# Kernel tuning notes

Hardware: AMD Instinct MI355X
Metric: run time of the kernel (lower is better)

## Reference

```python
import jax, jax.numpy as jnp
import numpy as np

NUM_HEADS = 8
DIM = 256
MLP_RATIO = 1.2


def conv1x1(x, w, b=None):
    # x: [B,C,H,W], w: [O,C]
    y = jnp.einsum('bchw,oc->bohw', x, w)
    if b is not None:
        y = y + b[None, :, None, None]
    return y


def dwconv3x3(x, w):
    # depthwise 3x3, stride 1, padding 1. w: [C,1,3,3]
    C = x.shape[1]
    return jax.lax.conv_general_dilated(
        x, w, window_strides=(1, 1), padding=((1, 1), (1, 1)),
        dimension_numbers=('NCHW', 'OIHW', 'NCHW'), feature_group_count=C)


def l2norm(x, axis):
    # matches torch.nn.functional.normalize (eps=1e-12 clamp on the norm)
    n = jnp.sqrt(jnp.sum(x * x, axis=axis, keepdims=True))
    return x / jnp.maximum(n, 1e-12)


def setup_inputs() -> dict:
    key = jax.random.key(0)
    ks = jax.random.split(key, 7)
    dim = DIM
    hidden = int(dim * MLP_RATIO)  # 307
    B, H, W = 8, 64, 64
    return {
        'x': jax.random.normal(ks[0], (B, dim, H, W), jnp.float32),
        'w_qkv': jax.random.normal(ks[1], (3 * dim, dim), jnp.float32) * 0.02,
        'w_dw': jax.random.normal(ks[2], (3 * dim, 1, 3, 3), jnp.float32) * 0.1,
        'temperature': jnp.ones((NUM_HEADS, 1, 1), jnp.float32),
        'w_proj': jax.random.normal(ks[3], (dim, dim), jnp.float32) * 0.02,
        'w_mlp1': jax.random.normal(ks[4], (hidden, dim), jnp.float32) * 0.02,
        'b_mlp1': jnp.zeros((hidden,), jnp.float32),
        'w_mlp2': jax.random.normal(ks[5], (dim, hidden), jnp.float32) * 0.02,
        'b_mlp2': jnp.zeros((dim,), jnp.float32),
    }


def reference(x, w_qkv, w_dw, temperature, w_proj, w_mlp1, b_mlp1, w_mlp2, b_mlp2):
    b, c, h, w = x.shape
    head = NUM_HEADS
    # MDTA attention: qkv 1x1 conv -> depthwise 3x3 conv
    qkv = dwconv3x3(conv1x1(x, w_qkv), w_dw)          # [B,3C,H,W]
    q, k, v = jnp.split(qkv, 3, axis=1)
    to_heads = lambda t: t.reshape(b, head, c // head, h * w)  # b head c (h w)
    q, k, v = to_heads(q), to_heads(k), to_heads(v)
    q = l2norm(q, -1)
    k = l2norm(k, -1)
    # channel-wise (transposed) attention: [B,head,c_h,c_h]
    attn = jnp.einsum('bhcn,bhdn->bhcd', q, k) * temperature[None]
    attn = jax.nn.softmax(attn, axis=-1)
    out = jnp.einsum('bhcd,bhdn->bhcn', attn, v).reshape(b, c, h, w)
    x = x + conv1x1(out, w_proj)                       # residual 1
    # conv-FFN (1x1 -> GELU -> 1x1) with residual
    y = jax.nn.gelu(conv1x1(x, w_mlp1, b_mlp1))
    x = x + conv1x1(y, w_mlp2, b_mlp2)                 # residual 2
    return x
```

## Files before the change

kernel.cpp:

```cpp
#include <hip/hip_runtime.h>
#include <hip/hip_bf16.h>
#include <math.h>

typedef __hip_bfloat16 bf16;
using s16x8 = __attribute__((ext_vector_type(8))) short;
using f32x4 = __attribute__((ext_vector_type(4))) float;

#define B_ 8
#define C_ 256
#define HW_ 4096
#define TC_ 768
#define NH_ 8
#define CH_ 32
#define HID_ 307
#define HIDP_ 320
#define HIDM_ 384

__device__ __forceinline__ float ldf(const float* p) { return *p; }
__device__ __forceinline__ float ldf(const bf16* p)  { return __bfloat162float(*p); }
__device__ __forceinline__ void  stf(float* p, float v) { *p = v; }
__device__ __forceinline__ void  stf(bf16* p, float v)  { *p = __float2bfloat16(v); }

__device__ __forceinline__ float gelu_tanh(float u) {
    float c = 0.7978845608028654f * (u + 0.044715f * u * u * u);
    return 0.5f * u * (1.f + tanhf(c));
}

__device__ __forceinline__ void stage16(const void* g, uint32_t* lbase, int lane) {
#if __has_builtin(__builtin_amdgcn_global_load_lds)
    __builtin_amdgcn_global_load_lds(
        (const __attribute__((address_space(1))) uint32_t*)g,
        (__attribute__((address_space(3))) uint32_t*)lbase, 16, 0, 0);
#else
    ((uint4*)lbase)[lane] = *(const uint4*)g;
#endif
}

template <typename TOut>
__global__ __launch_bounds__(256) void mfma_gemm(
    const bf16* __restrict__ A, const bf16* __restrict__ Xt,
    const float* __restrict__ bias, const float* __restrict__ res,
    TOut* __restrict__ out, int M, int N, int Kp, int act,
    size_t astride, size_t xstride, size_t ostride)
{
    int bt = blockIdx.z;
    A  += (size_t)bt * astride;
    Xt += (size_t)bt * xstride;
    out += (size_t)bt * ostride;
    if (res) res += (size_t)bt * ostride;
    int m0 = blockIdx.y * 128, n0 = blockIdx.x * 128;

    __shared__ uint32_t lds[8192];

    int tid = threadIdx.x;
    int w = tid >> 6, lane = tid & 63;
    int wr = w >> 1, wc = w & 1;
    int r15 = lane & 15, g = lane >> 4;

    f32x4 zero4 = {0.f, 0.f, 0.f, 0.f};
    f32x4 acc[4][4];
    #pragma unroll
    for (int i = 0; i < 4; i++)
        #pragma unroll
        for (int j = 0; j < 4; j++) acc[i][j] = zero4;

    int nkt = Kp >> 6;
    for (int kt = 0; kt < nkt; kt++) {
        #pragma unroll
        for (int i = 0; i < 4; i++) {
            int row = (w * 4 + i) * 8 + (lane >> 3);
            int us  = (lane & 7) ^ (row & 7);
            const bf16* sa = A  + (size_t)(m0 + row) * Kp + kt * 64 + us * 8;
            const bf16* sb = Xt + (size_t)(n0 + row) * Kp + kt * 64 + us * 8;
            stage16(sa, &lds[(w * 4 + i) * 256], lane);
            stage16(sb, &lds[4096 + (w * 4 + i) * 256], lane);
        }
        __syncthreads();

        s16x8 af[4][2], bfr[4][2];
        #pragma unroll
        for (int mm = 0; mm < 4; mm++) {
            int r = wr * 64 + mm * 16 + r15;
            #pragma unroll
            for (int ks = 0; ks < 2; ks++) {
                int u = (ks * 4 + g) ^ (r & 7);
                af[mm][ks] = *(const s16x8*)&lds[(unsigned)(r * 8 + u) * 4];
            }
        }
        #pragma unroll
        for (int nn = 0; nn < 4; nn++) {
            int r = wc * 64 + nn * 16 + r15;
            #pragma unroll
            for (int ks = 0; ks < 2; ks++) {
                int u = (ks * 4 + g) ^ (r & 7);
                bfr[nn][ks] = *(const s16x8*)&lds[4096 + (unsigned)(r * 8 + u) * 4];
            }
        }

        #pragma unroll
        for (int ks = 0; ks < 2; ks++)
            #pragma unroll
            for (int mm = 0; mm < 4; mm++)
                #pragma unroll
                for (int nn = 0; nn < 4; nn++)
                    acc[mm][nn] = __builtin_amdgcn_mfma_f32_16x16x32_bf16(
                        af[mm][ks], bfr[nn][ks], acc[mm][nn], 0, 0, 0);
        __syncthreads();
    }

    #pragma unroll
    for (int mm = 0; mm < 4; mm++) {
        int mbase = m0 + wr * 64 + mm * 16 + g * 4;
        #pragma unroll
        for (int rr = 0; rr < 4; rr++) {
            int m = mbase + rr;
            if (m >= M) continue;
            float bv = bias ? bias[m] : 0.f;
            #pragma unroll
            for (int nn = 0; nn < 4; nn++) {
                int n = n0 + wc * 64 + nn * 16 + r15;
                float v = acc[mm][nn][rr] + bv;
                if (act == 1) v = gelu_tanh(v);
                if (res) v += res[(size_t)m * N + n];
                stf(&out[(size_t)m * N + n], v);
            }
        }
    }
}

template <typename TIn>
__global__ __launch_bounds__(256) void transpose_kernel(
    const TIn* __restrict__ in, bf16* __restrict__ out,
    int R, int Ncols, int Rpad, size_t in_z, size_t out_z)
{
    in  += (size_t)blockIdx.z * in_z;
    out += (size_t)blockIdx.z * out_z;
    __shared__ float t[32][33];
    int r0 = blockIdx.y * 32, n0 = blockIdx.x * 32;
    int tx = threadIdx.x & 31, ty = threadIdx.x >> 5;
    #pragma unroll
    for (int s = 0; s < 4; s++) {
        int r = r0 + ty + 8 * s;
        t[ty + 8 * s][tx] = (r < R) ? ldf(&in[(size_t)r * Ncols + n0 + tx]) : 0.f;
    }
    __syncthreads();
    #pragma unroll
    for (int s = 0; s < 4; s++) {
        int n = n0 + ty + 8 * s;
        out[(size_t)n * Rpad + r0 + tx] = __float2bfloat16(t[tx][ty + 8 * s]);
    }
}

__global__ __launch_bounds__(256) void convert_pad_kernel(
    const float* __restrict__ in, bf16* __restrict__ out,
    int R, int Cin, int Cout)
{
    int c = blockIdx.x * 256 + threadIdx.x;
    int r = blockIdx.y;
    if (c >= Cout) return;
    float v = (r < R && c < Cin) ? in[(size_t)r * Cin + c] : 0.f;
    out[(size_t)r * Cout + c] = __float2bfloat16(v);
}

__global__ __launch_bounds__(256) void dwconv_kernel(
    const bf16* __restrict__ in, const float* __restrict__ wdw,
    bf16* __restrict__ out)
{
    size_t gid = (size_t)blockIdx.x * 256 + threadIdx.x;
    int pix  = (int)(gid & 4095);
    int xcol = pix & 63, yrow = pix >> 6;
    size_t plane = gid >> 12;
    int c = (int)(plane % TC_);
    const bf16* ip = in + (plane << 12);

    float wv[9];
    #pragma unroll
    for (int t = 0; t < 9; t++) wv[t] = wdw[c * 9 + t];

    float acc = 0.f;
    #pragma unroll
    for (int dy = -1; dy <= 1; dy++) {
        int yy = yrow + dy;
        if (yy < 0 || yy > 63) continue;
        #pragma unroll
        for (int dx = -1; dx <= 1; dx++) {
            int xx = xcol + dx;
            if (xx < 0 || xx > 63) continue;
            acc += wv[(dy + 1) * 3 + (dx + 1)] * __bfloat162float(ip[yy * 64 + xx]);
        }
    }
    out[gid] = __float2bfloat16(acc);
}

__global__ void zero_kernel(float* __restrict__ p, int n)
{
    int i = blockIdx.x * 256 + threadIdx.x;
    if (i < n) p[i] = 0.f;
}

__global__ __launch_bounds__(256) void qk_partial_kernel(
    const bf16* __restrict__ qkv, float* __restrict__ S,
    float* __restrict__ n2q, float* __restrict__ n2k)
{
    int bh = blockIdx.y;
    int b = bh >> 3, h = bh & 7;
    int base = blockIdx.x * 512;
    const bf16* qp = qkv + ((size_t)b * TC_ + h * CH_) * HW_;
    const bf16* kp = qp + (size_t)C_ * HW_;

    __shared__ float qs[32][65], ks[32][65];

    int tid = threadIdx.x;
    int nr = tid >> 3, seg = (tid & 7) * 8;
    float accA[4] = {0.f, 0.f, 0.f, 0.f};
    float sq = 0.f, sk = 0.f;

    for (int t0 = 0; t0 < 512; t0 += 64) {
        #pragma unroll
        for (int i = 0; i < 8; i++) {
            int l = tid + 256 * i;
            int r = l >> 6, cc = l & 63;
            qs[r][cc] = __bfloat162float(qp[(size_t)r * HW_ + base + t0 + cc]);
            ks[r][cc] = __bfloat162float(kp[(size_t)r * HW_ + base + t0 + cc]);
        }
        __syncthreads();
        #pragma unroll
        for (int p = 0; p < 4; p++) {
            int e = tid + 256 * p;
            int i = e >> 5, j = e & 31;
            float s = 0.f;
            #pragma unroll
            for (int kk = 0; kk < 64; kk++) s += qs[i][kk] * ks[j][kk];
            accA[p] += s;
        }
        #pragma unroll
        for (int s = 0; s < 8; s++) {
            float vq = qs[nr][seg + s]; sq += vq * vq;
            float vk = ks[nr][seg + s]; sk += vk * vk;
        }
        __syncthreads();
    }

    #pragma unroll
    for (int off = 1; off < 8; off <<= 1) {
        sq += __shfl_xor(sq, off);
        sk += __shfl_xor(sk, off);
    }
    if ((tid & 7) == 0) {
        atomicAdd(&n2q[bh * 32 + nr], sq);
        atomicAdd(&n2k[bh * 32 + nr], sk);
    }
    #pragma unroll
    for (int p = 0; p < 4; p++) {
        int e = tid + 256 * p;
        atomicAdd(&S[(size_t)bh * 1024 + e], accA[p]);
    }
}

__global__ __launch_bounds__(64) void softmax_kernel(
    const float* __restrict__ S, const float* __restrict__ n2q,
    const float* __restrict__ n2k, const float* __restrict__ temp,
    float* __restrict__ attnb)
{
    int bh = blockIdx.x, h = bh & 7;
    __shared__ float nkl[32];
    int tid = threadIdx.x;
    if (tid < 32) nkl[tid] = fmaxf(sqrtf(n2k[bh * 32 + tid]), 1e-12f);
    __syncthreads();
    if (tid < 32) {
        float nq = fmaxf(sqrtf(n2q[bh * 32 + tid]), 1e-12f);
        float tp = temp[h];
        float row[32];
        float m = -1e30f;
        #pragma unroll
        for (int j = 0; j < 32; j++) {
            row[j] = S[(size_t)bh * 1024 + tid * 32 + j] * tp / (nq * nkl[j]);
            m = fmaxf(m, row[j]);
        }
        float s = 0.f;
        #pragma unroll
        for (int j = 0; j < 32; j++) { row[j] = expf(row[j] - m); s += row[j]; }
        float inv = 1.f / s;
        #pragma unroll
        for (int j = 0; j < 32; j++)
            attnb[(size_t)bh * 1024 + tid * 32 + j] = row[j] * inv;
    }
}

__global__ __launch_bounds__(256) void wcomb_kernel(
    const float* __restrict__ w_proj, const float* __restrict__ attnb,
    bf16* __restrict__ wcomb)
{
    int bh = blockIdx.x;
    int b = bh >> 3, h = bh & 7;
    __shared__ float at[32][33];
    int tid = threadIdx.x;
    #pragma unroll
    for (int p = 0; p < 4; p++) {
        int e = tid + 256 * p;
        at[e >> 5][e & 31] = attnb[(size_t)bh * 1024 + e];
    }
    __syncthreads();
    int m = tid;
    float wrow[32];
    #pragma unroll
    for (int i = 0; i < 32; i++) wrow[i] = w_proj[(size_t)m * C_ + h * 32 + i];
    #pragma unroll
    for (int j = 0; j < 32; j++) {
        float s = 0.f;
        #pragma unroll
        for (int i = 0; i < 32; i++) s += wrow[i] * at[i][j];
        wcomb[((size_t)b * C_ + m) * C_ + h * 32 + j] = __float2bfloat16(s);
    }
}

extern "C" void kernel_launch(void* const* d_in, const int* in_sizes, int n_in,
                              void* d_out, int out_size, void* d_ws, size_t ws_size,
                              hipStream_t stream)
{
    const float* x      = (const float*)d_in[0];
    const float* w_qkv  = (const float*)d_in[1];
    const float* w_dw   = (const float*)d_in[2];
    const float* temp   = (const float*)d_in[3];
    const float* w_proj = (const float*)d_in[4];
    const float* w_mlp1 = (const float*)d_in[5];
    const float* b_mlp1 = (const float*)d_in[6];
    const float* w_mlp2 = (const float*)d_in[7];
    const float* b_mlp2 = (const float*)d_in[8];

    char* ws = (char*)d_ws;
    bf16*  qkv_pre = (bf16*)ws;
    bf16*  xt      = (bf16*)(ws + (size_t)50331648);
    bf16*  wqkv_bf = (bf16*)(ws + (size_t)67108864);
    bf16*  qkv     = (bf16*)(ws + (size_t)50331648);
    float* x2      = (float*)ws;
    float* S_f     = (float*)(ws + (size_t)33554432);
    float* n2q     = S_f + 65536;
    float* n2k     = n2q + 2048;
    float* attnb   = n2k + 2048;
    bf16*  wcomb   = (bf16*)(ws + (size_t)34095104);
    bf16*  wm1_bf  = (bf16*)(ws + (size_t)35143680);
    bf16*  wm2_bf  = (bf16*)(ws + (size_t)35340288);
    bf16*  vt      = (bf16*)(ws + (size_t)35504128);
    bf16*  ybuf    = (bf16*)(ws + (size_t)52281344);
    bf16*  x2t     = (bf16*)(ws + (size_t)72400896);
    bf16*  yt      = (bf16*)(ws + (size_t)72400896);

    convert_pad_kernel<<<dim3(1, TC_), 256, 0, stream>>>(w_qkv, wqkv_bf, TC_, C_, C_);
    transpose_kernel<float><<<dim3(128, 8, B_), 256, 0, stream>>>(
        x, xt, C_, HW_, C_, (size_t)C_ * HW_, (size_t)HW_ * C_);

    mfma_gemm<bf16><<<dim3(32, 6, B_), 256, 0, stream>>>(
        wqkv_bf, xt, nullptr, nullptr, qkv_pre, TC_, HW_, C_, 0,
        0, (size_t)HW_ * C_, (size_t)TC_ * HW_);

    dwconv_kernel<<<(B_ * TC_ * HW_) / 256, 256, 0, stream>>>(qkv_pre, w_dw, qkv);

    zero_kernel<<<(69632 + 255) / 256, 256, 0, stream>>>(S_f, 69632);
    qk_partial_kernel<<<dim3(8, 64), 256, 0, stream>>>(qkv, S_f, n2q, n2k);
    softmax_kernel<<<64, 64, 0, stream>>>(S_f, n2q, n2k, temp, attnb);
    wcomb_kernel<<<64, 256, 0, stream>>>(w_proj, attnb, wcomb);

    convert_pad_kernel<<<dim3(1, HIDM_), 256, 0, stream>>>(w_mlp1, wm1_bf, HID_, C_, C_);
    convert_pad_kernel<<<dim3(2, C_), 256, 0, stream>>>(w_mlp2, wm2_bf, C_, HID_, HIDP_);
    transpose_kernel<bf16><<<dim3(128, 8, B_), 256, 0, stream>>>(
        qkv + (size_t)2 * C_ * HW_, vt, C_, HW_, C_,
        (size_t)TC_ * HW_, (size_t)HW_ * C_);

    mfma_gemm<float><<<dim3(32, 2, B_), 256, 0, stream>>>(
        wcomb, vt, nullptr, x, x2, C_, HW_, C_, 0,
        (size_t)C_ * C_, (size_t)HW_ * C_, (size_t)C_ * HW_);

    transpose_kernel<float><<<dim3(128, 8, B_), 256, 0, stream>>>(
        x2, x2t, C_, HW_, C_, (size_t)C_ * HW_, (size_t)HW_ * C_);

    mfma_gemm<bf16><<<dim3(32, 3, B_), 256, 0, stream>>>(
        wm1_bf, x2t, b_mlp1, nullptr, ybuf, HID_, HW_, C_, 1,
        0, (size_t)HW_ * C_, (size_t)HID_ * HW_);

    transpose_kernel<bf16><<<dim3(128, 10, B_), 256, 0, stream>>>(
        ybuf, yt, HID_, HW_, HIDP_, (size_t)HID_ * HW_, (size_t)HW_ * HIDP_);

    mfma_gemm<float><<<dim3(32, 2, B_), 256, 0, stream>>>(
        wm2_bf, yt, b_mlp2, x2, (float*)d_out, C_, HW_, HIDP_, 0,
        0, (size_t)HW_ * HIDP_, (size_t)C_ * HW_);
}
```

Before: 443.8 us.

## Emit MLP1 output pre-transposed and tile depthwise conv through LDS

```diff
diff --git a/kernel.cpp b/kernel.cpp
--- a/kernel.cpp
+++ b/kernel.cpp
@@ -21,6 +21,10 @@
 __device__ __forceinline__ void  stf(float* p, float v) { *p = v; }
 __device__ __forceinline__ void  stf(bf16* p, float v)  { *p = __float2bfloat16(v); }
 
+__device__ __forceinline__ float bfu2f(unsigned short u) {
+    union { unsigned int i; float f; } c; c.i = ((unsigned int)u) << 16; return c.f;
+}
+
 __device__ __forceinline__ float gelu_tanh(float u) {
     float c = 0.7978845608028654f * (u + 0.044715f * u * u * u);
     return 0.5f * u * (1.f + tanhf(c));
@@ -40,7 +44,8 @@
 __global__ __launch_bounds__(256) void mfma_gemm(
     const bf16* __restrict__ A, const bf16* __restrict__ Xt,
     const float* __restrict__ bias, const float* __restrict__ res,
-    TOut* __restrict__ out, int M, int N, int Kp, int act,
+    TOut* __restrict__ out, int M, int Nld, int Nw, int Kp, int act,
+    int bias_on_n, int bias_len,
     size_t astride, size_t xstride, size_t ostride)
 {
     int bt = blockIdx.z;
@@ -115,14 +120,16 @@
         for (int rr = 0; rr < 4; rr++) {
             int m = mbase + rr;
             if (m >= M) continue;
-            float bv = bias ? bias[m] : 0.f;
+            float bvm = (bias && !bias_on_n) ? bias[m] : 0.f;
             #pragma unroll
             for (int nn = 0; nn < 4; nn++) {
                 int n = n0 + wc * 64 + nn * 16 + r15;
+                if (n >= Nw) continue;
+                float bv = bias_on_n ? ((bias && n < bias_len) ? bias[n] : 0.f) : bvm;
                 float v = acc[mm][nn][rr] + bv;
                 if (act == 1) v = gelu_tanh(v);
-                if (res) v += res[(size_t)m * N + n];
-                stf(&out[(size_t)m * N + n], v);
+                if (res) v += res[(size_t)m * Nld + n];
+                stf(&out[(size_t)m * Nld + n], v);
             }
         }
     }
@@ -166,30 +173,56 @@
     const bf16* __restrict__ in, const float* __restrict__ wdw,
     bf16* __restrict__ out)
 {
-    size_t gid = (size_t)blockIdx.x * 256 + threadIdx.x;
-    int pix  = (int)(gid & 4095);
-    int xcol = pix & 63, yrow = pix >> 6;
-    size_t plane = gid >> 12;
-    int c = (int)(plane % TC_);
-    const bf16* ip = in + (plane << 12);
-
-    float wv[9];
-    #pragma unroll
-    for (int t = 0; t < 9; t++) wv[t] = wdw[c * 9 + t];
-
-    float acc = 0.f;
+    int plane = blockIdx.x;
+    int c = plane % TC_;
+    const bf16* ip = in + ((size_t)plane << 12);
+    bf16*       op = out + ((size_t)plane << 12);
+
+    __shared__ bf16 sp[64][72];
+
+    int t = threadIdx.x;
+    #pragma unroll
+    for (int i = 0; i < 2; i++) {
+        int px = (t + 256 * i) * 8;
+        int r = px >> 6, col = px & 63;
+        *(uint4*)&sp[r][col] = *(const uint4*)&ip[px];
+    }
+    float w[9];
+    #pragma unroll
+    for (int k = 0; k < 9; k++) w[k] = wdw[c * 9 + k];
+    __syncthreads();
+
+    int row = t >> 2, c0 = (t & 3) * 16;
+    float acc[16];
+    #pragma unroll
+    for (int j = 0; j < 16; j++) acc[j] = 0.f;
+
     #pragma unroll
     for (int dy = -1; dy <= 1; dy++) {
-        int yy = yrow + dy;
+        int yy = row + dy;
         if (yy < 0 || yy > 63) continue;
-        #pragma unroll
-        for (int dx = -1; dx <= 1; dx++) {
-            int xx = xcol + dx;
-            if (xx < 0 || xx > 63) continue;
-            acc += wv[(dy + 1) * 3 + (dx + 1)] * __bfloat162float(ip[yy * 64 + xx]);
-        }
-    }
-    out[gid] = __float2bfloat16(acc);
+        float vals[18];
+        vals[0]  = (c0 > 0)       ? __bfloat162float(sp[yy][c0 - 1])  : 0.f;
+        s16x8 v0 = *(const s16x8*)&sp[yy][c0];
+        s16x8 v1 = *(const s16x8*)&sp[yy][c0 + 8];
+        #pragma unroll
+        for (int j = 0; j < 8; j++) {
+            vals[j + 1] = bfu2f((unsigned short)v0[j]);
+            vals[j + 9] = bfu2f((unsigned short)v1[j]);
+        }
+        vals[17] = (c0 + 16 < 64) ? __bfloat162float(sp[yy][c0 + 16]) : 0.f;
+        float w0 = w[(dy + 1) * 3], w1 = w[(dy + 1) * 3 + 1], w2 = w[(dy + 1) * 3 + 2];
+        #pragma unroll
+        for (int j = 0; j < 16; j++)
+            acc[j] += w0 * vals[j] + w1 * vals[j + 1] + w2 * vals[j + 2];
+    }
+
+    bf16 ob[16];
+    #pragma unroll
+    for (int j = 0; j < 16; j++) ob[j] = __float2bfloat16(acc[j]);
+    #pragma unroll
+    for (int i = 0; i < 2; i++)
+        *(uint4*)&op[row * 64 + c0 + i * 8] = *(uint4*)&ob[i * 8];
 }
 
 __global__ void zero_kernel(float* __restrict__ p, int n)
@@ -340,10 +373,9 @@
     float* attnb   = n2k + 2048;
     bf16*  wcomb   = (bf16*)(ws + (size_t)34095104);
     bf16*  wm1_bf  = (bf16*)(ws + (size_t)35143680);
-    bf16*  wm2_bf  = (bf16*)(ws + (size_t)35340288);
-    bf16*  vt      = (bf16*)(ws + (size_t)35504128);
-    bf16*  ybuf    = (bf16*)(ws + (size_t)52281344);
-    bf16*  x2t     = (bf16*)(ws + (size_t)72400896);
+    bf16*  wm2_bf  = (bf16*)(ws + (size_t)35438592);
+    bf16*  vt      = (bf16*)(ws + (size_t)35602432);
+    bf16*  x2t     = (bf16*)(ws + (size_t)52379648);
     bf16*  yt      = (bf16*)(ws + (size_t)72400896);
 
     convert_pad_kernel<<<dim3(1, TC_), 256, 0, stream>>>(w_qkv, wqkv_bf, TC_, C_, C_);
@@ -351,10 +383,10 @@
         x, xt, C_, HW_, C_, (size_t)C_ * HW_, (size_t)HW_ * C_);
 
     mfma_gemm<bf16><<<dim3(32, 6, B_), 256, 0, stream>>>(
-        wqkv_bf, xt, nullptr, nullptr, qkv_pre, TC_, HW_, C_, 0,
+        wqkv_bf, xt, nullptr, nullptr, qkv_pre, TC_, HW_, HW_, C_, 0, 0, 0,
         0, (size_t)HW_ * C_, (size_t)TC_ * HW_);
 
-    dwconv_kernel<<<(B_ * TC_ * HW_) / 256, 256, 0, stream>>>(qkv_pre, w_dw, qkv);
+    dwconv_kernel<<<B_ * TC_, 256, 0, stream>>>(qkv_pre, w_dw, qkv);
 
     zero_kernel<<<(69632 + 255) / 256, 256, 0, stream>>>(S_f, 69632);
     qk_partial_kernel<<<dim3(8, 64), 256, 0, stream>>>(qkv, S_f, n2q, n2k);
@@ -368,20 +400,17 @@
         (size_t)TC_ * HW_, (size_t)HW_ * C_);
 
     mfma_gemm<float><<<dim3(32, 2, B_), 256, 0, stream>>>(
-        wcomb, vt, nullptr, x, x2, C_, HW_, C_, 0,
+        wcomb, vt, nullptr, x, x2, C_, HW_, HW_, C_, 0, 0, 0,
         (size_t)C_ * C_, (size_t)HW_ * C_, (size_t)C_ * HW_);
 
     transpose_kernel<float><<<dim3(128, 8, B_), 256, 0, stream>>>(
         x2, x2t, C_, HW_, C_, (size_t)C_ * HW_, (size_t)HW_ * C_);
 
-    mfma_gemm<bf16><<<dim3(32, 3, B_), 256, 0, stream>>>(
-        wm1_bf, x2t, b_mlp1, nullptr, ybuf, HID_, HW_, C_, 1,
-        0, (size_t)HW_ * C_, (size_t)HID_ * HW_);
-
-    transpose_kernel<bf16><<<dim3(128, 10, B_), 256, 0, stream>>>(
-        ybuf, yt, HID_, HW_, HIDP_, (size_t)HID_ * HW_, (size_t)HW_ * HIDP_);
+    mfma_gemm<bf16><<<dim3(3, 32, B_), 256, 0, stream>>>(
+        x2t, wm1_bf, b_mlp1, nullptr, yt, HW_, HIDP_, HIDP_, C_, 1, 1, HID_,
+        (size_t)HW_ * C_, 0, (size_t)HW_ * HIDP_);
 
     mfma_gemm<float><<<dim3(32, 2, B_), 256, 0, stream>>>(
-        wm2_bf, yt, b_mlp2, x2, (float*)d_out, C_, HW_, HIDP_, 0,
+        wm2_bf, yt, b_mlp2, x2, (float*)d_out, C_, HW_, HW_, HIDP_, 0, 0, 0,
         0, (size_t)HW_ * HIDP_, (size_t)C_ * HW_);
 }
```

Result: faster. 377.7 us (-14.9%).
